# Kernel tuning notes

Measured on AMD Instinct MI355X. Metric: run time of the kernel, lower is better.

The kernel has to match this reference:

```python
import jax, jax.numpy as jnp
import numpy as np
from jax import lax

LEAK = 0.9
THRESHOLD = 1.0
SLOPE = 5.0


def setup_inputs() -> dict:
    key = jax.random.key(0)
    k1, _ = jax.random.split(key)
    current = jax.random.normal(k1, (8, 4096, 1024), dtype=jnp.float32)
    membrane = jnp.zeros((8, 1024), dtype=jnp.float32)
    return {"current": current, "membrane": membrane}


def reference(current, membrane):
    """LIF neuron: V = leak*V + I; spike = (V >= theta); V -= spike*theta.
    Spike uses a straight-through surrogate (sigmoid derivative) for grads.
    current: [B, S, D], membrane: [B, D].
    """
    def step(mem, cur_t):
        mem = LEAK * mem + cur_t                       # integrate with leak
        sg = jax.nn.sigmoid(SLOPE * (mem - THRESHOLD)) # surrogate (grad path)
        hard = (mem >= THRESHOLD).astype(mem.dtype)    # hard spike (fwd value)
        spike = sg + lax.stop_gradient(hard - sg)      # value=hard, grad=d(sg)
        mem = mem - spike * THRESHOLD                  # soft reset
        return mem, spike

    cur_t_first = jnp.swapaxes(current, 0, 1)          # [S, B, D]
    mem_final, spikes = lax.scan(step, membrane, cur_t_first)
    spikes = jnp.swapaxes(spikes, 0, 1)                # [B, S, D]
    return spikes, mem_final
```

## Files before the change

kernel.cpp:

```cpp
#include <hip/hip_runtime.h>


#define LIF_B 8
#define LIF_S 4096
#define LIF_D 1024
#define CHUNK 256
#define NH    (LIF_S / CHUNK)
#define CPB   64

typedef __attribute__((address_space(3))) unsigned int lds_uint;
typedef const __attribute__((address_space(1))) unsigned int glb_uint;

__device__ __forceinline__ void stage_chunk(const float* gwin, int tb,
                                            int prow, int pcol,
                                            float* slotbase) {
    #pragma unroll
    for (int f = 0; f < CHUNK / 4; ++f) {
        const float* src = gwin + (size_t)(tb + 4 * f + prow) * LIF_D + pcol;
        __builtin_amdgcn_global_load_lds(
            (glb_uint*)(const void*)src,
            (lds_uint*)(void*)(slotbase + (size_t)4 * f * 64), 16, 0, 0);
    }
}

__global__ __launch_bounds__(256, 1) void lif_v10_kernel(
    const float* __restrict__ current,
    const float* __restrict__ membrane,
    float* __restrict__ spikes,
    float* __restrict__ mem_out)
{
    #pragma clang fp contract(off)

    __shared__ __align__(16) float in_ring[2][CHUNK][CPB];
    __shared__ unsigned mask_lds[2][8][CPB];

    const int wid  = threadIdx.x >> 6;
    const int lane = threadIdx.x & 63;
    const int blk  = blockIdx.x;
    const int bb   = blk >> 4;
    const int ch0  = (blk & 15) * CPB;

    const float* gwin  = current + (size_t)bb * LIF_S * LIF_D + ch0;
    float*       sbase = spikes  + (size_t)bb * LIF_S * LIF_D + ch0;

    const int prow = lane >> 4;
    const int pcol = (lane & 15) * 4;

    float mem = 0.0f;

    if (wid == 1) {
        stage_chunk(gwin, 0, prow, pcol, &in_ring[0][0][0]);
        asm volatile("s_waitcnt vmcnt(0)" ::: "memory");
    } else if (wid == 0) {
        mem = membrane[bb * LIF_D + ch0 + lane];
    }
    __builtin_amdgcn_s_barrier();
    asm volatile("" ::: "memory");

    for (int h = 0; h < NH; ++h) {
        if (wid == 0) {
            const float* ib = &in_ring[h & 1][0][lane];
            unsigned m[8];
            #pragma unroll
            for (int j = 0; j < 8; ++j) m[j] = 0u;

            float A[16], Bv[16];
            #pragma unroll
            for (int j = 0; j < 16; ++j) A[j]  = ib[j * CPB];
            #pragma unroll
            for (int j = 0; j < 16; ++j) Bv[j] = ib[(16 + j) * CPB];

            #pragma unroll
            for (int b = 0; b < 16; ++b) {
                const int wd = b >> 1;
                const int sh = (b & 1) * 16;
                #pragma unroll
                for (int j = 0; j < 16; ++j) {
                    const float c = ((b & 1) == 0) ? A[j] : Bv[j];
                    const float v = 0.9f * mem + c;
                    const float w = v - 1.0f;
                    const bool  f = (v >= 1.0f);
                    m[wd] |= f ? (1u << (sh + j)) : 0u;
                    mem = f ? w : v;
                }
                if (b + 2 < 16) {
                    #pragma unroll
                    for (int j = 0; j < 16; ++j) {
                        if ((b & 1) == 0) A[j]  = ib[((b + 2) * 16 + j) * CPB];
                        else              Bv[j] = ib[((b + 2) * 16 + j) * CPB];
                    }
                }
            }

            #pragma unroll
            for (int j = 0; j < 8; ++j)
                mask_lds[h & 1][j][lane] = m[j];
            asm volatile("s_waitcnt lgkmcnt(0)" ::: "memory");
        } else if (wid == 1) {
            if (h + 1 < NH) {
                stage_chunk(gwin, (h + 1) * CHUNK, prow, pcol,
                            &in_ring[(h + 1) & 1][0][0]);
                asm volatile("s_waitcnt vmcnt(0)" ::: "memory");
            }
        } else {
            if (h >= 1) {
                const int tb = (h - 1) * CHUNK;
                const unsigned* mw = &mask_lds[(h - 1) & 1][0][0];
                const int wbase = (wid == 3) ? 4 : 0;
                const int rbase = (wid == 3) ? 128 : 0;
                unsigned M[4][4];
                #pragma unroll
                for (int c = 0; c < 4; ++c)
                    #pragma unroll
                    for (int w = 0; w < 4; ++w)
                        M[c][w] = mw[(wbase + w) * CPB + pcol + c];
                #pragma unroll
                for (int k = 0; k < 32; ++k) {
                    const int widx = k >> 3;
                    const unsigned bit = (unsigned)(((4 * k) & 31) + prow);
                    float4 vv;
                    vv.x = ((M[0][widx] >> bit) & 1u) ? 1.0f : 0.0f;
                    vv.y = ((M[1][widx] >> bit) & 1u) ? 1.0f : 0.0f;
                    vv.z = ((M[2][widx] >> bit) & 1u) ? 1.0f : 0.0f;
                    vv.w = ((M[3][widx] >> bit) & 1u) ? 1.0f : 0.0f;
                    const int tl = rbase + 4 * k + prow;
                    *(float4*)(sbase + (size_t)(tb + tl) * LIF_D + pcol) = vv;
                }
                asm volatile("s_waitcnt lgkmcnt(0)" ::: "memory");
            }
        }
        __builtin_amdgcn_s_barrier();
        asm volatile("" ::: "memory");
    }

    if (wid >= 2) {
        const int tb = (NH - 1) * CHUNK;
        const unsigned* mw = &mask_lds[(NH - 1) & 1][0][0];
        const int wbase = (wid == 3) ? 4 : 0;
        const int rbase = (wid == 3) ? 128 : 0;
        unsigned M[4][4];
        #pragma unroll
        for (int c = 0; c < 4; ++c)
            #pragma unroll
            for (int w = 0; w < 4; ++w)
                M[c][w] = mw[(wbase + w) * CPB + pcol + c];
        #pragma unroll
        for (int k = 0; k < 32; ++k) {
            const int widx = k >> 3;
            const unsigned bit = (unsigned)(((4 * k) & 31) + prow);
            float4 vv;
            vv.x = ((M[0][widx] >> bit) & 1u) ? 1.0f : 0.0f;
            vv.y = ((M[1][widx] >> bit) & 1u) ? 1.0f : 0.0f;
            vv.z = ((M[2][widx] >> bit) & 1u) ? 1.0f : 0.0f;
            vv.w = ((M[3][widx] >> bit) & 1u) ? 1.0f : 0.0f;
            const int tl = rbase + 4 * k + prow;
            *(float4*)(sbase + (size_t)(tb + tl) * LIF_D + pcol) = vv;
        }
    } else if (wid == 0) {
        mem_out[bb * LIF_D + ch0 + lane] = mem;
    }
}

extern "C" void kernel_launch(void* const* d_in, const int* in_sizes, int n_in,
                              void* d_out, int out_size, void* d_ws, size_t ws_size,
                              hipStream_t stream) {
    const float* current  = (const float*)d_in[0];
    const float* membrane = (const float*)d_in[1];

    float* spikes  = (float*)d_out;
    float* mem_out = (float*)d_out + (size_t)LIF_B * LIF_S * LIF_D;

    dim3 block(256);
    dim3 grid(LIF_B * LIF_D / CPB);

    hipLaunchKernelGGL(lif_v10_kernel, grid, block, 0, stream,
                       current, membrane, spikes, mem_out);
}
```

Before: 75.23 us.

## Halve channels per block and split scan across two consumer waves

Halves the channels per block from 64 to 32, which doubles the grid to 256 blocks so every CU can get one. Each block grows to 8 waves: two consumer waves scan 16 channels each, two producers split the async global-to-LDS staging, and four writer waves expand the spike bitmasks. The aim is to spread the latency-bound serial recurrence and the memory traffic over more CUs and more independent dependency chains. In exchange, consumer waves use only 16 of 64 lanes usefully, and per-block memory work is spread over more waves.

```diff
diff --git a/kernel.cpp b/kernel.cpp
--- a/kernel.cpp
+++ b/kernel.cpp
@@ -6,24 +6,12 @@
 #define LIF_D 1024
 #define CHUNK 256
 #define NH    (LIF_S / CHUNK)
-#define CPB   64
+#define CPB   32
 
 typedef __attribute__((address_space(3))) unsigned int lds_uint;
 typedef const __attribute__((address_space(1))) unsigned int glb_uint;
 
-__device__ __forceinline__ void stage_chunk(const float* gwin, int tb,
-                                            int prow, int pcol,
-                                            float* slotbase) {
-    #pragma unroll
-    for (int f = 0; f < CHUNK / 4; ++f) {
-        const float* src = gwin + (size_t)(tb + 4 * f + prow) * LIF_D + pcol;
-        __builtin_amdgcn_global_load_lds(
-            (glb_uint*)(const void*)src,
-            (lds_uint*)(void*)(slotbase + (size_t)4 * f * 64), 16, 0, 0);
-    }
-}
-
-__global__ __launch_bounds__(256, 1) void lif_v10_kernel(
+__global__ __launch_bounds__(512, 1) void lif_v13_kernel(
     const float* __restrict__ current,
     const float* __restrict__ membrane,
     float* __restrict__ spikes,
@@ -37,29 +25,44 @@
     const int wid  = threadIdx.x >> 6;
     const int lane = threadIdx.x & 63;
     const int blk  = blockIdx.x;
-    const int bb   = blk >> 4;
-    const int ch0  = (blk & 15) * CPB;
+    const int bb   = blk >> 5;
+    const int ch0  = (blk & 31) * CPB;
 
     const float* gwin  = current + (size_t)bb * LIF_S * LIF_D + ch0;
     float*       sbase = spikes  + (size_t)bb * LIF_S * LIF_D + ch0;
 
-    const int prow = lane >> 4;
-    const int pcol = (lane & 15) * 4;
+    const int prow = lane >> 3;
+    const int pcol = (lane & 7) * 4;
+    const int lx   = lane & 15;
+
+    const bool is_cons = (wid == 0) || (wid == 4);
+    const bool is_prod = (wid == 1) || (wid == 5);
+    const int  co      = (wid == 4) ? 16 : 0;
+    const int  phalf   = (wid == 5) ? 1 : 0;
+    const int  wi      = (wid == 2) ? 0 : (wid == 3) ? 1 : (wid == 6) ? 2 : 3;
 
     float mem = 0.0f;
 
-    if (wid == 1) {
-        stage_chunk(gwin, 0, prow, pcol, &in_ring[0][0][0]);
+    if (is_prod) {
+        #pragma unroll
+        for (int f = 0; f < 16; ++f) {
+            const float* src = gwin
+                + (size_t)(phalf * 128 + 8 * f + prow) * LIF_D + pcol;
+            __builtin_amdgcn_global_load_lds(
+                (glb_uint*)(const void*)src,
+                (lds_uint*)(void*)(&in_ring[0][0][0]
+                                   + (size_t)(phalf * 16 + f) * 256), 16, 0, 0);
+        }
         asm volatile("s_waitcnt vmcnt(0)" ::: "memory");
-    } else if (wid == 0) {
-        mem = membrane[bb * LIF_D + ch0 + lane];
+    } else if (is_cons) {
+        mem = membrane[bb * LIF_D + ch0 + co + lx];
     }
     __builtin_amdgcn_s_barrier();
     asm volatile("" ::: "memory");
 
     for (int h = 0; h < NH; ++h) {
-        if (wid == 0) {
-            const float* ib = &in_ring[h & 1][0][lane];
+        if (is_cons) {
+            const float* ib = &in_ring[h & 1][0][co + lx];
             unsigned m[8];
             #pragma unroll
             for (int j = 0; j < 8; ++j) m[j] = 0u;
@@ -92,39 +95,50 @@
                 }
             }
 
-            #pragma unroll
-            for (int j = 0; j < 8; ++j)
-                mask_lds[h & 1][j][lane] = m[j];
+            if (lane < 16) {
+                #pragma unroll
+                for (int j = 0; j < 8; ++j)
+                    mask_lds[h & 1][j][co + lane] = m[j];
+            }
             asm volatile("s_waitcnt lgkmcnt(0)" ::: "memory");
-        } else if (wid == 1) {
+        } else if (is_prod) {
             if (h + 1 < NH) {
-                stage_chunk(gwin, (h + 1) * CHUNK, prow, pcol,
-                            &in_ring[(h + 1) & 1][0][0]);
+                const int tb = (h + 1) * CHUNK;
+                #pragma unroll
+                for (int f = 0; f < 16; ++f) {
+                    const float* src = gwin
+                        + (size_t)(tb + phalf * 128 + 8 * f + prow) * LIF_D + pcol;
+                    __builtin_amdgcn_global_load_lds(
+                        (glb_uint*)(const void*)src,
+                        (lds_uint*)(void*)(&in_ring[(h + 1) & 1][0][0]
+                                           + (size_t)(phalf * 16 + f) * 256),
+                        16, 0, 0);
+                }
                 asm volatile("s_waitcnt vmcnt(0)" ::: "memory");
             }
         } else {
             if (h >= 1) {
+                const int ph = (h - 1) & 1;
                 const int tb = (h - 1) * CHUNK;
-                const unsigned* mw = &mask_lds[(h - 1) & 1][0][0];
-                const int wbase = (wid == 3) ? 4 : 0;
-                const int rbase = (wid == 3) ? 128 : 0;
-                unsigned M[4][4];
+                const int whalf = lane >> 5;
+                const int wIdx  = 2 * wi + whalf;
+                const int c4    = lane & 7;
+                const int rsub  = (lane >> 3) & 3;
+                const int rb    = wi * 64 + whalf * 32;
+                unsigned M[4];
                 #pragma unroll
                 for (int c = 0; c < 4; ++c)
-                    #pragma unroll
-                    for (int w = 0; w < 4; ++w)
-                        M[c][w] = mw[(wbase + w) * CPB + pcol + c];
+                    M[c] = mask_lds[ph][wIdx][4 * c4 + c];
                 #pragma unroll
-                for (int k = 0; k < 32; ++k) {
-                    const int widx = k >> 3;
-                    const unsigned bit = (unsigned)(((4 * k) & 31) + prow);
+                for (int k = 0; k < 8; ++k) {
+                    const int rloc = rsub * 8 + k;
+                    const int row  = rb + rloc;
                     float4 vv;
-                    vv.x = ((M[0][widx] >> bit) & 1u) ? 1.0f : 0.0f;
-                    vv.y = ((M[1][widx] >> bit) & 1u) ? 1.0f : 0.0f;
-                    vv.z = ((M[2][widx] >> bit) & 1u) ? 1.0f : 0.0f;
-                    vv.w = ((M[3][widx] >> bit) & 1u) ? 1.0f : 0.0f;
-                    const int tl = rbase + 4 * k + prow;
-                    *(float4*)(sbase + (size_t)(tb + tl) * LIF_D + pcol) = vv;
+                    vv.x = (float)((M[0] >> rloc) & 1u);
+                    vv.y = (float)((M[1] >> rloc) & 1u);
+                    vv.z = (float)((M[2] >> rloc) & 1u);
+                    vv.w = (float)((M[3] >> rloc) & 1u);
+                    *(float4*)(sbase + (size_t)(tb + row) * LIF_D + 4 * c4) = vv;
                 }
                 asm volatile("s_waitcnt lgkmcnt(0)" ::: "memory");
             }
@@ -133,31 +147,31 @@
         asm volatile("" ::: "memory");
     }
 
-    if (wid >= 2) {
+    if (!is_cons && !is_prod) {
+        const int ph = (NH - 1) & 1;
         const int tb = (NH - 1) * CHUNK;
-        const unsigned* mw = &mask_lds[(NH - 1) & 1][0][0];
-        const int wbase = (wid == 3) ? 4 : 0;
-        const int rbase = (wid == 3) ? 128 : 0;
-        unsigned M[4][4];
+        const int whalf = lane >> 5;
+        const int wIdx  = 2 * wi + whalf;
+        const int c4    = lane & 7;
+        const int rsub  = (lane >> 3) & 3;
+        const int rb    = wi * 64 + whalf * 32;
+        unsigned M[4];
         #pragma unroll
         for (int c = 0; c < 4; ++c)
-            #pragma unroll
-            for (int w = 0; w < 4; ++w)
-                M[c][w] = mw[(wbase + w) * CPB + pcol + c];
+            M[c] = mask_lds[ph][wIdx][4 * c4 + c];
         #pragma unroll
-        for (int k = 0; k < 32; ++k) {
-            const int widx = k >> 3;
-            const unsigned bit = (unsigned)(((4 * k) & 31) + prow);
+        for (int k = 0; k < 8; ++k) {
+            const int rloc = rsub * 8 + k;
+            const int row  = rb + rloc;
             float4 vv;
-            vv.x = ((M[0][widx] >> bit) & 1u) ? 1.0f : 0.0f;
-            vv.y = ((M[1][widx] >> bit) & 1u) ? 1.0f : 0.0f;
-            vv.z = ((M[2][widx] >> bit) & 1u) ? 1.0f : 0.0f;
-            vv.w = ((M[3][widx] >> bit) & 1u) ? 1.0f : 0.0f;
-            const int tl = rbase + 4 * k + prow;
-            *(float4*)(sbase + (size_t)(tb + tl) * LIF_D + pcol) = vv;
+            vv.x = (float)((M[0] >> rloc) & 1u);
+            vv.y = (float)((M[1] >> rloc) & 1u);
+            vv.z = (float)((M[2] >> rloc) & 1u);
+            vv.w = (float)((M[3] >> rloc) & 1u);
+            *(float4*)(sbase + (size_t)(tb + row) * LIF_D + 4 * c4) = vv;
         }
-    } else if (wid == 0) {
-        mem_out[bb * LIF_D + ch0 + lane] = mem;
+    } else if (is_cons && lane < 16) {
+        mem_out[bb * LIF_D + ch0 + co + lane] = mem;
     }
 }
 
@@ -170,9 +184,9 @@
     float* spikes  = (float*)d_out;
     float* mem_out = (float*)d_out + (size_t)LIF_B * LIF_S * LIF_D;
 
-    dim3 block(256);
+    dim3 block(512);
     dim3 grid(LIF_B * LIF_D / CPB);
 
-    hipLaunchKernelGGL(lif_v10_kernel, grid, block, 0, stream,
+    hipLaunchKernelGGL(lif_v13_kernel, grid, block, 0, stream,
                        current, membrane, spikes, mem_out);
 }
```

After: 144.1 us. +91.5%, slower.

## Shrink channels per block to 16 to launch four times more blocks

Applied to the files above, without the earlier changes.

Cuts the channels each block handles from 64 to 16, so the grid grows from 128 to 512 blocks and spreads the serial LIF scan across more CUs. The staging loads and the spike-writeback indexing are rewritten for 16-column rows (64-byte row segments), and the writeback now reads the mask words directly from LDS instead of preloading them into registers. The risk is that three quarters of the compute wave's lanes are idle and that 64-byte global accesses coalesce less well than 256-byte ones.

```diff
diff --git a/kernel.cpp b/kernel.cpp
--- a/kernel.cpp
+++ b/kernel.cpp
@@ -6,24 +6,24 @@
 #define LIF_D 1024
 #define CHUNK 256
 #define NH    (LIF_S / CHUNK)
-#define CPB   64
+#define CPB   16
 
 typedef __attribute__((address_space(3))) unsigned int lds_uint;
 typedef const __attribute__((address_space(1))) unsigned int glb_uint;
 
-__device__ __forceinline__ void stage_chunk(const float* gwin, int tb,
-                                            int prow, int pcol,
-                                            float* slotbase) {
+__device__ __forceinline__ void stage_chunk16(const float* gwin, int tb,
+                                              int prow, int pcol,
+                                              float* slotbase) {
     #pragma unroll
-    for (int f = 0; f < CHUNK / 4; ++f) {
-        const float* src = gwin + (size_t)(tb + 4 * f + prow) * LIF_D + pcol;
+    for (int f = 0; f < CHUNK / 16; ++f) {
+        const float* src = gwin + (size_t)(tb + 16 * f + prow) * LIF_D + pcol;
         __builtin_amdgcn_global_load_lds(
             (glb_uint*)(const void*)src,
-            (lds_uint*)(void*)(slotbase + (size_t)4 * f * 64), 16, 0, 0);
+            (lds_uint*)(void*)(slotbase + (size_t)f * 256), 16, 0, 0);
     }
 }
 
-__global__ __launch_bounds__(256, 1) void lif_v10_kernel(
+__global__ __launch_bounds__(256, 1) void lif_v16_kernel(
     const float* __restrict__ current,
     const float* __restrict__ membrane,
     float* __restrict__ spikes,
@@ -37,21 +37,22 @@
     const int wid  = threadIdx.x >> 6;
     const int lane = threadIdx.x & 63;
     const int blk  = blockIdx.x;
-    const int bb   = blk >> 4;
-    const int ch0  = (blk & 15) * CPB;
+    const int bb   = blk >> 6;
+    const int ch0  = (blk & 63) * CPB;
 
     const float* gwin  = current + (size_t)bb * LIF_S * LIF_D + ch0;
     float*       sbase = spikes  + (size_t)bb * LIF_S * LIF_D + ch0;
 
-    const int prow = lane >> 4;
-    const int pcol = (lane & 15) * 4;
+    const int prow = lane >> 2;
+    const int pcol = (lane & 3) * 4;
+    const int lx   = lane & 15;
 
     float mem = 0.0f;
 
     if (wid == 1) {
-        stage_chunk(gwin, 0, prow, pcol, &in_ring[0][0][0]);
+        stage_chunk16(gwin, 0, prow, pcol, &in_ring[0][0][0]);
         asm volatile("s_waitcnt vmcnt(0)" ::: "memory");
-    } else if (wid == 0) {
+    } else if (wid == 0 && lane < CPB) {
         mem = membrane[bb * LIF_D + ch0 + lane];
     }
     __builtin_amdgcn_s_barrier();
@@ -59,7 +60,7 @@
 
     for (int h = 0; h < NH; ++h) {
         if (wid == 0) {
-            const float* ib = &in_ring[h & 1][0][lane];
+            const float* ib = &in_ring[h & 1][0][lx];
             unsigned m[8];
             #pragma unroll
             for (int j = 0; j < 8; ++j) m[j] = 0u;
@@ -92,39 +93,36 @@
                 }
             }
 
-            #pragma unroll
-            for (int j = 0; j < 8; ++j)
-                mask_lds[h & 1][j][lane] = m[j];
+            if (lane < CPB) {
+                #pragma unroll
+                for (int j = 0; j < 8; ++j)
+                    mask_lds[h & 1][j][lane] = m[j];
+            }
             asm volatile("s_waitcnt lgkmcnt(0)" ::: "memory");
         } else if (wid == 1) {
             if (h + 1 < NH) {
-                stage_chunk(gwin, (h + 1) * CHUNK, prow, pcol,
-                            &in_ring[(h + 1) & 1][0][0]);
+                stage_chunk16(gwin, (h + 1) * CHUNK, prow, pcol,
+                              &in_ring[(h + 1) & 1][0][0]);
                 asm volatile("s_waitcnt vmcnt(0)" ::: "memory");
             }
         } else {
             if (h >= 1) {
+                const int ph = (h - 1) & 1;
                 const int tb = (h - 1) * CHUNK;
-                const unsigned* mw = &mask_lds[(h - 1) & 1][0][0];
-                const int wbase = (wid == 3) ? 4 : 0;
+                const int rgrp = lane >> 2;
+                const int c4   = lane & 3;
                 const int rbase = (wid == 3) ? 128 : 0;
-                unsigned M[4][4];
                 #pragma unroll
-                for (int c = 0; c < 4; ++c)
-                    #pragma unroll
-                    for (int w = 0; w < 4; ++w)
-                        M[c][w] = mw[(wbase + w) * CPB + pcol + c];
-                #pragma unroll
-                for (int k = 0; k < 32; ++k) {
-                    const int widx = k >> 3;
-                    const unsigned bit = (unsigned)(((4 * k) & 31) + prow);
+                for (int k = 0; k < 8; ++k) {
+                    const int row = rbase + k * 16 + rgrp;
+                    const int wIdx = row >> 5;
+                    const int bit  = row & 31;
                     float4 vv;
-                    vv.x = ((M[0][widx] >> bit) & 1u) ? 1.0f : 0.0f;
-                    vv.y = ((M[1][widx] >> bit) & 1u) ? 1.0f : 0.0f;
-                    vv.z = ((M[2][widx] >> bit) & 1u) ? 1.0f : 0.0f;
-                    vv.w = ((M[3][widx] >> bit) & 1u) ? 1.0f : 0.0f;
-                    const int tl = rbase + 4 * k + prow;
-                    *(float4*)(sbase + (size_t)(tb + tl) * LIF_D + pcol) = vv;
+                    vv.x = (float)((mask_lds[ph][wIdx][4 * c4 + 0] >> bit) & 1u);
+                    vv.y = (float)((mask_lds[ph][wIdx][4 * c4 + 1] >> bit) & 1u);
+                    vv.z = (float)((mask_lds[ph][wIdx][4 * c4 + 2] >> bit) & 1u);
+                    vv.w = (float)((mask_lds[ph][wIdx][4 * c4 + 3] >> bit) & 1u);
+                    *(float4*)(sbase + (size_t)(tb + row) * LIF_D + 4 * c4) = vv;
                 }
                 asm volatile("s_waitcnt lgkmcnt(0)" ::: "memory");
             }
@@ -134,29 +132,24 @@
     }
 
     if (wid >= 2) {
+        const int ph = (NH - 1) & 1;
         const int tb = (NH - 1) * CHUNK;
-        const unsigned* mw = &mask_lds[(NH - 1) & 1][0][0];
-        const int wbase = (wid == 3) ? 4 : 0;
+        const int rgrp = lane >> 2;
+        const int c4   = lane & 3;
         const int rbase = (wid == 3) ? 128 : 0;
-        unsigned M[4][4];
         #pragma unroll
-        for (int c = 0; c < 4; ++c)
-            #pragma unroll
-            for (int w = 0; w < 4; ++w)
-                M[c][w] = mw[(wbase + w) * CPB + pcol + c];
-        #pragma unroll
-        for (int k = 0; k < 32; ++k) {
-            const int widx = k >> 3;
-            const unsigned bit = (unsigned)(((4 * k) & 31) + prow);
+        for (int k = 0; k < 8; ++k) {
+            const int row = rbase + k * 16 + rgrp;
+            const int wIdx = row >> 5;
+            const int bit  = row & 31;
             float4 vv;
-            vv.x = ((M[0][widx] >> bit) & 1u) ? 1.0f : 0.0f;
-            vv.y = ((M[1][widx] >> bit) & 1u) ? 1.0f : 0.0f;
-            vv.z = ((M[2][widx] >> bit) & 1u) ? 1.0f : 0.0f;
-            vv.w = ((M[3][widx] >> bit) & 1u) ? 1.0f : 0.0f;
-            const int tl = rbase + 4 * k + prow;
-            *(float4*)(sbase + (size_t)(tb + tl) * LIF_D + pcol) = vv;
+            vv.x = (float)((mask_lds[ph][wIdx][4 * c4 + 0] >> bit) & 1u);
+            vv.y = (float)((mask_lds[ph][wIdx][4 * c4 + 1] >> bit) & 1u);
+            vv.z = (float)((mask_lds[ph][wIdx][4 * c4 + 2] >> bit) & 1u);
+            vv.w = (float)((mask_lds[ph][wIdx][4 * c4 + 3] >> bit) & 1u);
+            *(float4*)(sbase + (size_t)(tb + row) * LIF_D + 4 * c4) = vv;
         }
-    } else if (wid == 0) {
+    } else if (wid == 0 && lane < CPB) {
         mem_out[bb * LIF_D + ch0 + lane] = mem;
     }
 }
@@ -173,6 +166,6 @@
     dim3 block(256);
     dim3 grid(LIF_B * LIF_D / CPB);
 
-    hipLaunchKernelGGL(lif_v10_kernel, grid, block, 0, stream,
+    hipLaunchKernelGGL(lif_v16_kernel, grid, block, 0, stream,
                        current, membrane, spikes, mem_out);
 }
```

New measurement: 124.7 us. +65.8%, slower.
